# Performance work log

Hardware: AMD Instinct MI355X
Metric: run time of the kernel (lower is better)

The kernel has to match this reference:

```python
import jax, jax.numpy as jnp
import numpy as np

NUM_EXPERTS = 32
TOP_K = 8
SELECT_TOP_K = 4
THRESHOLD = 0.5
HIDDEN = 2048
D_FF = 768


def setup_inputs() -> dict:
    key = jax.random.key(0)
    ks = jax.random.split(key, 5)
    hidden_states = jax.random.normal(ks[0], (4, 2048, HIDDEN), dtype=jnp.float32)
    gate_weight = jax.random.normal(ks[1], (NUM_EXPERTS, HIDDEN), dtype=jnp.float32) * 0.02
    gate_up_proj = jax.random.normal(ks[2], (NUM_EXPERTS, 2 * D_FF, HIDDEN), dtype=jnp.float32) * 0.02
    down_proj = jax.random.normal(ks[3], (NUM_EXPERTS, HIDDEN, D_FF), dtype=jnp.float32) * 0.02
    similarity = jax.random.uniform(ks[4], (NUM_EXPERTS, NUM_EXPERTS), dtype=jnp.float32)
    return {
        "hidden_states": hidden_states,
        "gate_weight": gate_weight,
        "gate_up_proj": gate_up_proj,
        "down_proj": down_proj,
        "similarity": similarity,
    }


def _moe_forward(hidden_states, gate_weight, gate_up_proj, down_proj, similarity):
    B, S_len, H = hidden_states.shape
    E, K, Ssel = NUM_EXPERTS, TOP_K, SELECT_TOP_K
    x = hidden_states.reshape(-1, H)  # [T, H]

    # Router: logits -> fp32 softmax -> top-k -> renormalize
    router_logits = x @ gate_weight.T  # [T, E]
    router_probs = jax.nn.softmax(router_logits.astype(jnp.float32), axis=-1).astype(router_logits.dtype)
    router_top_value, router_indices = jax.lax.top_k(router_probs, K)  # [T, K]
    routing_weights = router_top_value / jnp.clip(
        jnp.sum(router_top_value, axis=-1, keepdims=True), 1e-12, None
    )

    # SERE rerouting: map each secondary expert to its most-similar primary expert
    sim = similarity.astype(jnp.float32)
    sim = sim.at[jnp.arange(E), jnp.arange(E)].set(1.0)  # fill_diagonal_(1.0)
    prim = router_indices[:, :Ssel]            # [T, S]
    sec = router_indices[:, Ssel:]             # [T, K-S]
    sim_cand = sim[sec[:, :, None], prim[:, None, :]]        # [T, K-S, S]
    best_sim = jnp.max(sim_cand, axis=-1)                    # [T, K-S]
    best_i = jnp.argmax(sim_cand, axis=-1)                   # [T, K-S]
    prim_rep = jnp.broadcast_to(prim[:, None, :], sim_cand.shape)
    best_primary = jnp.take_along_axis(prim_rep, best_i[..., None], axis=-1)[..., 0]
    new_sec = jnp.where(best_sim < THRESHOLD, sec, best_primary) if THRESHOLD > 0.0 else best_primary
    rerouted_indices = jnp.concatenate([prim, new_sec], axis=1)  # [T, K]

    # Combine weights per (token, expert); duplicate expert slots accumulate (index_add semantics)
    combine = jnp.sum(
        jax.nn.one_hot(rerouted_indices, E, dtype=routing_weights.dtype)
        * routing_weights[..., None],
        axis=1,
    )  # [T, E]

    # Dense masked expert sweep (scan over experts keeps peak memory at one [T, 2*D_FF] buffer)
    def expert_step(y, params):
        wgu, wd, cw = params  # [2F, H], [H, F], [T]
        gu = x @ wgu.T                      # [T, 2F]
        g, u = jnp.split(gu, 2, axis=-1)
        h = jax.nn.silu(g) * u              # SwiGLU
        y = y + (h @ wd.T) * cw[:, None]
        return y, None

    y0 = jnp.zeros_like(x)
    y, _ = jax.lax.scan(expert_step, y0, (gate_up_proj, down_proj, combine.T))
    return y.reshape(B, S_len, H)


def reference(hidden_states, gate_weight, gate_up_proj, down_proj, similarity):
    return _moe_forward(hidden_states, gate_weight, gate_up_proj, down_proj, similarity)
```

## Files before the change

### kernel.cpp

```cpp
#include <hip/hip_runtime.h>
#include <stdint.h>
#include <string.h>

#define NTOK 8192
#define HID 2048
#define NE 32
#define DFF 768
#define NSLOT 65536
#define NB 256
#define MT 256
#define MAX_TILES 288

typedef unsigned short u16;
typedef unsigned int u32;

using f32x4 = __attribute__((ext_vector_type(4))) float;
using bf16x8 = __attribute__((ext_vector_type(8))) short;

static __device__ __forceinline__ u16 f2bf(float f) {
  u32 x = __float_as_uint(f);
  x += 0x7fffu + ((x >> 16) & 1u);
  return (u16)(x >> 16);
}

typedef const __attribute__((address_space(1))) unsigned int* gp_t;
typedef __attribute__((address_space(3))) unsigned int* lp_t;
static __device__ __forceinline__ void gload16(const void* g, void* l) {
  __builtin_amdgcn_global_load_lds((gp_t)g, (lp_t)l, 16, 0, 0);
}

__global__ void convert2_kernel(const float* __restrict__ s1, u16* __restrict__ d1, int n1,
                                const float* __restrict__ s2, u16* __restrict__ d2, int n2) {
  int i = blockIdx.x * blockDim.x + threadIdx.x;
  int stride = gridDim.x * blockDim.x;
  int total = n1 + n2;
  for (; i < total; i += stride) {
    const float* src = (i < n1) ? s1 : s2;
    u16* dst = (i < n1) ? d1 : d2;
    int k = (i < n1) ? i : (i - n1);
    float4 v = reinterpret_cast<const float4*>(src)[k];
    u32 lo = (u32)f2bf(v.x) | ((u32)f2bf(v.y) << 16);
    u32 hi = (u32)f2bf(v.z) | ((u32)f2bf(v.w) << 16);
    reinterpret_cast<uint2*>(dst)[k] = make_uint2(lo, hi);
  }
}

__global__ void router_kernel(const float* __restrict__ x, const float* __restrict__ gw,
                              const float* __restrict__ sim,
                              int* __restrict__ slot_e, float* __restrict__ slot_w,
                              u16* __restrict__ xb) {
  int t = blockIdx.x;
  __shared__ float xs[HID];
  __shared__ float logits[NE];
  const float* xr = x + (size_t)t * HID;
  for (int i = threadIdx.x; i < HID / 4; i += 256)
    reinterpret_cast<float4*>(xs)[i] = reinterpret_cast<const float4*>(xr)[i];
  __syncthreads();
  {
    int i = threadIdx.x;
    float4 v0 = reinterpret_cast<float4*>(xs)[i * 2];
    float4 v1 = reinterpret_cast<float4*>(xs)[i * 2 + 1];
    uint4 o;
    o.x = (u32)f2bf(v0.x) | ((u32)f2bf(v0.y) << 16);
    o.y = (u32)f2bf(v0.z) | ((u32)f2bf(v0.w) << 16);
    o.z = (u32)f2bf(v1.x) | ((u32)f2bf(v1.y) << 16);
    o.w = (u32)f2bf(v1.z) | ((u32)f2bf(v1.w) << 16);
    reinterpret_cast<uint4*>(xb + (size_t)t * HID)[i] = o;
  }
  int e = threadIdx.x >> 3, part = threadIdx.x & 7;
  const float4* wv = reinterpret_cast<const float4*>(gw + (size_t)e * HID + part * 256);
  const float4* xv = reinterpret_cast<const float4*>(xs + part * 256);
  float s = 0.f;
#pragma unroll
  for (int j = 0; j < 64; ++j) {
    float4 a = xv[j], b = wv[j];
    s += a.x * b.x + a.y * b.y + a.z * b.z + a.w * b.w;
  }
  s += __shfl_xor(s, 1); s += __shfl_xor(s, 2); s += __shfl_xor(s, 4);
  if (part == 0) logits[e] = s;
  __syncthreads();
  if (threadIdx.x < 64) {
    int lane = threadIdx.x;
    float myv = (lane < NE) ? logits[lane] : -3.4e38f;
    int myi = lane;
    float cur = myv;
    int idx[8]; float lv[8];
#pragma unroll
    for (int k = 0; k < 8; ++k) {
      float bv = cur; int bi = myi;
#pragma unroll
      for (int off = 32; off; off >>= 1) {
        float ov = __shfl_xor(bv, off);
        int oi = __shfl_xor(bi, off);
        if (ov > bv || (ov == bv && oi < bi)) { bv = ov; bi = oi; }
      }
      idx[k] = bi; lv[k] = bv;
      if (myi == bi) cur = -3.4e38f;
    }
    float w[8]; float ssum = 0.f;
#pragma unroll
    for (int k = 0; k < 8; ++k) { w[k] = __expf(lv[k] - lv[0]); ssum += w[k]; }
    float inv = 1.f / ssum;
    int base = t * 8;
    if (lane < 4) {
      slot_e[base + lane] = idx[lane];
      slot_w[base + lane] = w[lane] * inv;
      int sj = idx[4 + lane];
      float best = -2.f; int bsel = idx[0];
#pragma unroll
      for (int i = 0; i < 4; ++i) {
        int pe = idx[i];
        float sv = sim[sj * NE + pe];
        bool ok = sv > best;
        best = ok ? sv : best;
        bsel = ok ? pe : bsel;
      }
      int ns = (best < 0.5f) ? sj : bsel;
      slot_e[base + 4 + lane] = ns;
      slot_w[base + 4 + lane] = w[4 + lane] * inv;
    }
  }
}

__global__ void hist_kernel(const int* __restrict__ slot_e, int* __restrict__ blockCounts) {
  __shared__ int cnt[NE];
  if (threadIdx.x < NE) cnt[threadIdx.x] = 0;
  __syncthreads();
  int i = blockIdx.x * 256 + threadIdx.x;
  atomicAdd(&cnt[slot_e[i]], 1);
  __syncthreads();
  if (threadIdx.x < NE) blockCounts[threadIdx.x * NB + blockIdx.x] = cnt[threadIdx.x];
}

__global__ void scan_kernel(const int* __restrict__ blockCounts, int* __restrict__ startEB,
                            int* __restrict__ tile_e, int* __restrict__ tile_row0,
                            int* __restrict__ tile_cnt, int* __restrict__ tileCount) {
  __shared__ int totals[NE];
  __shared__ int bases[NE];
  int t = threadIdx.x;
  if (t < NE) {
    int run = 0;
    for (int b = 0; b < NB; ++b) run += blockCounts[t * NB + b];
    totals[t] = run;
  }
  __syncthreads();
  if (t == 0) {
    int base = 0, nt = 0;
    for (int e = 0; e < NE; ++e) {
      bases[e] = base;
      int tot = totals[e];
      for (int i = 0; i < tot; i += MT) {
        tile_e[nt] = e;
        tile_row0[nt] = base + i;
        tile_cnt[nt] = (tot - i < MT) ? (tot - i) : MT;
        ++nt;
      }
      base += tot;
    }
    *tileCount = nt;
  }
  __syncthreads();
  if (t < NE) {
    int run = bases[t];
    for (int b = 0; b < NB; ++b) {
      startEB[t * NB + b] = run;
      run += blockCounts[t * NB + b];
    }
  }
}

__global__ void place_kernel(const int* __restrict__ slot_e, const float* __restrict__ slot_w,
                             const int* __restrict__ startEB,
                             int* __restrict__ perm_token, float* __restrict__ perm_w,
                             int* __restrict__ inv) {
  __shared__ int se[256];
  __shared__ float sw[256];
  int b = blockIdx.x;
  for (int i = threadIdx.x; i < 256; i += 64) {
    se[i] = slot_e[b * 256 + i];
    sw[i] = slot_w[b * 256 + i];
  }
  __syncthreads();
  int e = threadIdx.x;
  if (e < NE) {
    int pos = startEB[e * NB + b];
    for (int i = 0; i < 256; ++i) {
      if (se[i] == e) {
        perm_token[pos] = (b * 256 + i) >> 3;
        perm_w[pos] = sw[i];
        inv[b * 256 + i] = pos;
        ++pos;
      }
    }
  }
}


#define GUMM(AR, M_)                                                                   \
  acc[M_][0] = __builtin_amdgcn_mfma_f32_16x16x32_bf16(AR, b0, acc[M_][0], 0, 0, 0);   \
  acc[M_][1] = __builtin_amdgcn_mfma_f32_16x16x32_bf16(AR, b1, acc[M_][1], 0, 0, 0);   \
  acc[M_][2] = __builtin_amdgcn_mfma_f32_16x16x32_bf16(AR, b2, acc[M_][2], 0, 0, 0);   \
  acc[M_][3] = __builtin_amdgcn_mfma_f32_16x16x32_bf16(AR, b3, acc[M_][3], 0, 0, 0);

#define GWIN(BUF, KK, VM, S1, S2)                                                      \
  do {                                                                                 \
    asm volatile("s_waitcnt lgkmcnt(0)" ::: "memory");                                 \
    __builtin_amdgcn_sched_barrier(0);                                                 \
    asm volatile("s_waitcnt vmcnt(" #VM ")" ::: "memory");                             \
    __builtin_amdgcn_s_barrier();                                                      \
    const u16* Ap_ = &SA[BUF][KK][abase];                                              \
    const u16* Bp_ = &SB[BUF][KK][0];                                                  \
    bf16x8 a0_ = *(const bf16x8*)(Ap_);                                                \
    bf16x8 a1_ = *(const bf16x8*)(Ap_ + 512);                                          \
    bf16x8 a2_ = *(const bf16x8*)(Ap_ + 1024);                                         \
    bf16x8 a3_ = *(const bf16x8*)(Ap_ + 1536);                                         \
    bf16x8 b0 = *(const bf16x8*)(Bp_ + boff0);                                         \
    bf16x8 b1 = *(const bf16x8*)(Bp_ + boff1);                                         \
    bf16x8 b2 = *(const bf16x8*)(Bp_ + boff2);                                         \
    bf16x8 b3 = *(const bf16x8*)(Bp_ + boff3);                                         \
    S1;                                                                                \
    __builtin_amdgcn_s_setprio(1);                                                     \
    GUMM(a0_, 0) GUMM(a1_, 1) GUMM(a2_, 2) GUMM(a3_, 3)                                \
    __builtin_amdgcn_s_setprio(0);                                                     \
    bf16x8 c0_ = *(const bf16x8*)(Ap_ + 2048);                                         \
    bf16x8 c1_ = *(const bf16x8*)(Ap_ + 2560);                                         \
    bf16x8 c2_ = *(const bf16x8*)(Ap_ + 3072);                                         \
    bf16x8 c3_ = *(const bf16x8*)(Ap_ + 3584);                                         \
    S2;                                                                                \
    __builtin_amdgcn_s_setprio(1);                                                     \
    GUMM(c0_, 4) GUMM(c1_, 5) GUMM(c2_, 6) GUMM(c3_, 7)                                \
    __builtin_amdgcn_s_setprio(0);                                                     \
  } while (0)

__global__ __launch_bounds__(512, 2) void gu_fast(
    const u16* __restrict__ xb, const u16* __restrict__ wgub,
    const int* __restrict__ perm_token,
    const int* __restrict__ tile_e, const int* __restrict__ tile_row0,
    const int* __restrict__ tile_cnt, const int* __restrict__ tileCount,
    u16* __restrict__ h_perm) {
  int flat = blockIdx.x + blockIdx.y * 6;
  int xcd = flat & 7;
  int j = flat >> 3;
  int tile = xcd * 36 + j / 6;
  int n0g = (j % 6) * 128;
  if (tile >= *tileCount) return;
  int e = tile_e[tile], row0 = tile_row0[tile], cnt = tile_cnt[tile];
  __shared__ __align__(16) u16 SA[2][2][8192];
  __shared__ __align__(16) u16 SB[2][2][8192];
  __shared__ int toks[256];
  int tid = threadIdx.x;
  if (tid < 256) {
    int idx = row0 + tid;
    if (idx > NSLOT - 1) idx = NSLOT - 1;
    toks[tid] = perm_token[idx];
  }
  __syncthreads();
  int wave = tid >> 6, lane = tid & 63;
  int wr = wave >> 2, wc = wave & 3;
  int lr = lane & 15, lk = lane >> 4;
  int sr0 = tid >> 2;
  int sc0 = (tid & 3) ^ ((tid >> 3) & 3);
  const u16* gA0 = xb + (size_t)toks[sr0] * HID + sc0 * 8;
  const u16* gA1 = xb + (size_t)toks[128 + sr0] * HID + sc0 * 8;
  const u16* wgb = wgub + (size_t)e * (2 * DFF) * HID;
  const u16* gB0 = wgb + (size_t)(n0g + sr0) * HID + sc0 * 8;
  const u16* gB1 = wgb + (size_t)(DFF + n0g + sr0) * HID + sc0 * 8;
  int d0 = tid * 8, d1 = 4096 + tid * 8;

  int slot8 = (lk ^ ((lr >> 1) & 3)) * 8;
  int abase = (wr * 128 + lr) * 32 + slot8;
  int boff0 = (wc * 32 + 0 * 16 + lr) * 32 + slot8;
  int boff1 = (wc * 32 + 1 * 16 + lr) * 32 + slot8;
  int boff2 = (128 + wc * 32 + 0 * 16 + lr) * 32 + slot8;
  int boff3 = (128 + wc * 32 + 1 * 16 + lr) * 32 + slot8;

  f32x4 acc[8][4];
  f32x4 zero = {0.f, 0.f, 0.f, 0.f};
#pragma unroll
  for (int m = 0; m < 8; ++m)
#pragma unroll
    for (int n = 0; n < 4; ++n) acc[m][n] = zero;

#define GU_SGA(BUF, KK, KT) do { \
    gload16(gA0 + (KT) + (KK) * 32, &SA[BUF][KK][d0]); \
    gload16(gA1 + (KT) + (KK) * 32, &SA[BUF][KK][d1]); } while (0)
#define GU_SGB(BUF, KK, KT) do { \
    gload16(gB0 + (KT) + (KK) * 32, &SB[BUF][KK][d0]); \
    gload16(gB1 + (KT) + (KK) * 32, &SB[BUF][KK][d1]); } while (0)

  GU_SGA(0, 0, 0); GU_SGB(0, 0, 0);
  GU_SGA(0, 1, 0); GU_SGB(0, 1, 0);
  GU_SGA(1, 0, 64); GU_SGB(1, 0, 64);

  const int NKT = HID / 64;
  const int NI = NKT / 2;
  for (int it = 0; it < NI - 1; ++it) {
    int ktA = (2 * it + 1) * 64;
    int ktB = (2 * it + 2) * 64;
    int ktC = (2 * it + 3) * 64;
    GWIN(0, 0, 8, GU_SGA(1, 1, ktA), GU_SGB(1, 1, ktA));
    GWIN(0, 1, 8, GU_SGA(0, 0, ktB), GU_SGB(0, 0, ktB));
    GWIN(1, 0, 8, GU_SGA(0, 1, ktB), GU_SGB(0, 1, ktB));
    GWIN(1, 1, 8, GU_SGA(1, 0, ktC), GU_SGB(1, 0, ktC));
  }
  {
    int ktA = (2 * (NI - 1) + 1) * 64;
    GWIN(0, 0, 8, GU_SGA(1, 1, ktA), GU_SGB(1, 1, ktA));
    GWIN(0, 1, 8, (void)0, (void)0);
    GWIN(1, 0, 4, (void)0, (void)0);
    GWIN(1, 1, 0, (void)0, (void)0);
  }

#pragma unroll
  for (int m = 0; m < 8; ++m)
#pragma unroll
    for (int i = 0; i < 4; ++i) {
      int row = wr * 128 + m * 16 + lk * 4 + i;
      if (row < cnt) {
#pragma unroll
        for (int nf = 0; nf < 2; ++nf) {
          int col = n0g + wc * 32 + nf * 16 + lr;
          float g = acc[m][nf][i], u = acc[m][nf + 2][i];
          float h = g / (1.f + __expf(-g)) * u;
          h_perm[(size_t)(row0 + row) * DFF + col] = f2bf(h);
        }
      }
    }
#undef GU_SGA
#undef GU_SGB
}

__global__ __launch_bounds__(512, 2) void down_fast(
    const u16* __restrict__ h_perm, const u16* __restrict__ wdb,
    const float* __restrict__ perm_w,
    const int* __restrict__ tile_e, const int* __restrict__ tile_row0,
    const int* __restrict__ tile_cnt, const int* __restrict__ tileCount,
    _Float16* __restrict__ yp) {
  int flat = blockIdx.x + blockIdx.y * 8;
  int xcd = flat & 7;
  int j = flat >> 3;
  int tile = xcd * 36 + j / 8;
  int n0 = (j % 8) * 256;
  if (tile >= *tileCount) return;
  int e = tile_e[tile], row0 = tile_row0[tile], cnt = tile_cnt[tile];
  __shared__ __align__(16) u16 SA[2][2][8192];
  __shared__ __align__(16) u16 SB[2][2][8192];
  __shared__ float wts[256];
  int tid = threadIdx.x;
  if (tid < 256) {
    int idx = row0 + tid;
    if (idx > NSLOT - 1) idx = NSLOT - 1;
    wts[tid] = perm_w[idx];
  }
  __syncthreads();
  int wave = tid >> 6, lane = tid & 63;
  int wr = wave >> 2, wc = wave & 3;
  int lr = lane & 15, lk = lane >> 4;
  int sr0 = tid >> 2;
  int sc0 = (tid & 3) ^ ((tid >> 3) & 3);
  int ia0 = row0 + sr0;       if (ia0 > NSLOT - 1) ia0 = NSLOT - 1;
  int ia1 = row0 + 128 + sr0; if (ia1 > NSLOT - 1) ia1 = NSLOT - 1;
  const u16* gA0 = h_perm + (size_t)ia0 * DFF + sc0 * 8;
  const u16* gA1 = h_perm + (size_t)ia1 * DFF + sc0 * 8;
  const u16* wb = wdb + (size_t)e * HID * DFF;
  const u16* gB0 = wb + (size_t)(n0 + sr0) * DFF + sc0 * 8;
  const u16* gB1 = wb + (size_t)(n0 + 128 + sr0) * DFF + sc0 * 8;
  int d0 = tid * 8, d1 = 4096 + tid * 8;

  int slot8 = (lk ^ ((lr >> 1) & 3)) * 8;
  int abase = (wr * 128 + lr) * 32 + slot8;
  int boff0 = (wc * 64 + 0 * 16 + lr) * 32 + slot8;
  int boff1 = (wc * 64 + 1 * 16 + lr) * 32 + slot8;
  int boff2 = (wc * 64 + 2 * 16 + lr) * 32 + slot8;
  int boff3 = (wc * 64 + 3 * 16 + lr) * 32 + slot8;

  f32x4 acc[8][4];
  f32x4 zero = {0.f, 0.f, 0.f, 0.f};
#pragma unroll
  for (int m = 0; m < 8; ++m)
#pragma unroll
    for (int n = 0; n < 4; ++n) acc[m][n] = zero;

#define DN_SGA(BUF, KK, KT) do { \
    gload16(gA0 + (KT) + (KK) * 32, &SA[BUF][KK][d0]); \
    gload16(gA1 + (KT) + (KK) * 32, &SA[BUF][KK][d1]); } while (0)
#define DN_SGB(BUF, KK, KT) do { \
    gload16(gB0 + (KT) + (KK) * 32, &SB[BUF][KK][d0]); \
    gload16(gB1 + (KT) + (KK) * 32, &SB[BUF][KK][d1]); } while (0)

  DN_SGA(0, 0, 0); DN_SGB(0, 0, 0);
  DN_SGA(0, 1, 0); DN_SGB(0, 1, 0);
  DN_SGA(1, 0, 64); DN_SGB(1, 0, 64);

  const int NKT = DFF / 64;
  const int NI = NKT / 2;
  for (int it = 0; it < NI - 1; ++it) {
    int ktA = (2 * it + 1) * 64;
    int ktB = (2 * it + 2) * 64;
    int ktC = (2 * it + 3) * 64;
    GWIN(0, 0, 8, DN_SGA(1, 1, ktA), DN_SGB(1, 1, ktA));
    GWIN(0, 1, 8, DN_SGA(0, 0, ktB), DN_SGB(0, 0, ktB));
    GWIN(1, 0, 8, DN_SGA(0, 1, ktB), DN_SGB(0, 1, ktB));
    GWIN(1, 1, 8, DN_SGA(1, 0, ktC), DN_SGB(1, 0, ktC));
  }
  {
    int ktA = (2 * (NI - 1) + 1) * 64;
    GWIN(0, 0, 8, DN_SGA(1, 1, ktA), DN_SGB(1, 1, ktA));
    GWIN(0, 1, 8, (void)0, (void)0);
    GWIN(1, 0, 4, (void)0, (void)0);
    GWIN(1, 1, 0, (void)0, (void)0);
  }

#pragma unroll
  for (int m = 0; m < 8; ++m)
#pragma unroll
    for (int i = 0; i < 4; ++i) {
      int row = wr * 128 + m * 16 + lk * 4 + i;
      if (row < cnt) {
        float wt = wts[row];
#pragma unroll
        for (int nf = 0; nf < 4; ++nf) {
          int col = n0 + wc * 64 + nf * 16 + lr;
          yp[(size_t)(row0 + row) * HID + col] = (_Float16)(acc[m][nf][i] * wt);
        }
      }
    }
#undef DN_SGA
#undef DN_SGB
}

__global__ void reduce_kernel(const _Float16* __restrict__ yp, const int* __restrict__ inv,
                              float* __restrict__ y) {
  int t = blockIdx.x;
  __shared__ int pos[8];
  if (threadIdx.x < 8) pos[threadIdx.x] = inv[t * 8 + threadIdx.x];
  __syncthreads();
  int c = threadIdx.x * 8;
  float s[8] = {0.f, 0.f, 0.f, 0.f, 0.f, 0.f, 0.f, 0.f};
#pragma unroll
  for (int j = 0; j < 8; ++j) {
    uint4 v = *reinterpret_cast<const uint4*>(yp + (size_t)pos[j] * HID + c);
    const u16* p = reinterpret_cast<const u16*>(&v);
#pragma unroll
    for (int k = 0; k < 8; ++k) {
      _Float16 h;
      u16 us = p[k];
      __builtin_memcpy(&h, &us, 2);
      s[k] += (float)h;
    }
  }
  float* yo = y + (size_t)t * HID + c;
  float4 o0 = {s[0], s[1], s[2], s[3]};
  float4 o1 = {s[4], s[5], s[6], s[7]};
  *reinterpret_cast<float4*>(yo) = o0;
  *reinterpret_cast<float4*>(yo + 4) = o1;
}

extern "C" void kernel_launch(void* const* d_in, const int* in_sizes, int n_in,
                              void* d_out, int out_size, void* d_ws, size_t ws_size,
                              hipStream_t stream) {
  const float* x = (const float*)d_in[0];
  const float* gw = (const float*)d_in[1];
  const float* wgu = (const float*)d_in[2];
  const float* wd = (const float*)d_in[3];
  const float* sim = (const float*)d_in[4];
  float* y = (float*)d_out;

  char* ws = (char*)d_ws;
  size_t off = 0;
  auto alloc = [&](size_t bytes) {
    char* p = ws + off;
    off += (bytes + 255) & ~(size_t)255;
    return p;
  };
  u16* xb = (u16*)alloc((size_t)NTOK * HID * 2);
  u16* h_perm = (u16*)alloc((size_t)NSLOT * DFF * 2);
  int* slot_e = (int*)alloc(NSLOT * 4);
  float* slot_w = (float*)alloc(NSLOT * 4);
  int* perm_token = (int*)alloc(NSLOT * 4);
  float* perm_w = (float*)alloc(NSLOT * 4);
  int* inv = (int*)alloc(NSLOT * 4);
  int* blockCounts = (int*)alloc(NE * NB * 4);
  int* startEB = (int*)alloc(NE * NB * 4);
  int* tile_e = (int*)alloc(MAX_TILES * 4);
  int* tile_row0 = (int*)alloc(MAX_TILES * 4);
  int* tile_cnt = (int*)alloc(MAX_TILES * 4);
  int* tileCount = (int*)alloc(4);

  size_t wgu_elems = (size_t)NE * 2 * DFF * HID;
  size_t wd_elems = (size_t)NE * HID * DFF;
  size_t region_bytes = (size_t)NSLOT * HID * 2;
  u16* wd_b = (u16*)alloc(wd_elems * 2);
  char* region = alloc(region_bytes);
  u16* wgu_b = (u16*)region;
  _Float16* yp = (_Float16*)region;
  if (off > ws_size) return;

  router_kernel<<<NTOK, 256, 0, stream>>>(x, gw, sim, slot_e, slot_w, xb);
  hist_kernel<<<NB, 256, 0, stream>>>(slot_e, blockCounts);
  scan_kernel<<<1, 64, 0, stream>>>(blockCounts, startEB, tile_e, tile_row0, tile_cnt, tileCount);
  place_kernel<<<NB, 64, 0, stream>>>(slot_e, slot_w, startEB, perm_token, perm_w, inv);

  convert2_kernel<<<8192, 256, 0, stream>>>(wgu, wgu_b, (int)(wgu_elems / 4),
                                            wd, wd_b, (int)(wd_elems / 4));
  gu_fast<<<dim3(DFF / 128, MAX_TILES), 512, 0, stream>>>(
      xb, wgu_b, perm_token, tile_e, tile_row0, tile_cnt, tileCount, h_perm);
  down_fast<<<dim3(HID / 256, MAX_TILES), 512, 0, stream>>>(
      h_perm, wd_b, perm_w, tile_e, tile_row0, tile_cnt, tileCount, yp);
  reduce_kernel<<<NTOK, 256, 0, stream>>>(yp, inv, y);
}
```

Baseline: 1.205 ms.

## Fuse router, histogram and weight conversion into one kernel launch

Measured after the change: 1.211 ms. Within noise of the previous version (+0.5%).

```diff
diff --git a/kernel.cpp b/kernel.cpp
--- a/kernel.cpp
+++ b/kernel.cpp
@@ -10,6 +10,7 @@
 #define NB 256
 #define MT 256
 #define MAX_TILES 288
+#define CVT_BLOCKS 4096
 
 typedef unsigned short u16;
 typedef unsigned int u32;
@@ -29,29 +30,30 @@
   __builtin_amdgcn_global_load_lds((gp_t)g, (lp_t)l, 16, 0, 0);
 }
 
-__global__ void convert2_kernel(const float* __restrict__ s1, u16* __restrict__ d1, int n1,
-                                const float* __restrict__ s2, u16* __restrict__ d2, int n2) {
-  int i = blockIdx.x * blockDim.x + threadIdx.x;
-  int stride = gridDim.x * blockDim.x;
-  int total = n1 + n2;
-  for (; i < total; i += stride) {
-    const float* src = (i < n1) ? s1 : s2;
-    u16* dst = (i < n1) ? d1 : d2;
-    int k = (i < n1) ? i : (i - n1);
-    float4 v = reinterpret_cast<const float4*>(src)[k];
-    u32 lo = (u32)f2bf(v.x) | ((u32)f2bf(v.y) << 16);
-    u32 hi = (u32)f2bf(v.z) | ((u32)f2bf(v.w) << 16);
-    reinterpret_cast<uint2*>(dst)[k] = make_uint2(lo, hi);
-  }
-}
-
-__global__ void router_kernel(const float* __restrict__ x, const float* __restrict__ gw,
-                              const float* __restrict__ sim,
-                              int* __restrict__ slot_e, float* __restrict__ slot_w,
-                              u16* __restrict__ xb) {
-  int t = blockIdx.x;
+__global__ void router_convert_kernel(const float* __restrict__ x, const float* __restrict__ gw,
+                                      const float* __restrict__ sim,
+                                      int* __restrict__ slot_e, float* __restrict__ slot_w,
+                                      u16* __restrict__ xb, int* __restrict__ blockCounts,
+                                      const float* __restrict__ wgu, u16* __restrict__ wgu_b, int n1,
+                                      const float* __restrict__ wd, u16* __restrict__ wd_b, int n2) {
   __shared__ float xs[HID];
   __shared__ float logits[NE];
+  if (blockIdx.x >= NTOK) {
+    int i = (blockIdx.x - NTOK) * 256 + threadIdx.x;
+    int stride = CVT_BLOCKS * 256;
+    int total = n1 + n2;
+    for (; i < total; i += stride) {
+      const float* src = (i < n1) ? wgu : wd;
+      u16* dst = (i < n1) ? wgu_b : wd_b;
+      int k = (i < n1) ? i : (i - n1);
+      float4 v = reinterpret_cast<const float4*>(src)[k];
+      u32 lo = (u32)f2bf(v.x) | ((u32)f2bf(v.y) << 16);
+      u32 hi = (u32)f2bf(v.z) | ((u32)f2bf(v.w) << 16);
+      reinterpret_cast<uint2*>(dst)[k] = make_uint2(lo, hi);
+    }
+    return;
+  }
+  int t = blockIdx.x;
   const float* xr = x + (size_t)t * HID;
   for (int i = threadIdx.x; i < HID / 4; i += 256)
     reinterpret_cast<float4*>(xs)[i] = reinterpret_cast<const float4*>(xr)[i];
@@ -118,18 +120,10 @@
       int ns = (best < 0.5f) ? sj : bsel;
       slot_e[base + 4 + lane] = ns;
       slot_w[base + 4 + lane] = w[4 + lane] * inv;
-    }
-  }
-}
-
-__global__ void hist_kernel(const int* __restrict__ slot_e, int* __restrict__ blockCounts) {
-  __shared__ int cnt[NE];
-  if (threadIdx.x < NE) cnt[threadIdx.x] = 0;
-  __syncthreads();
-  int i = blockIdx.x * 256 + threadIdx.x;
-  atomicAdd(&cnt[slot_e[i]], 1);
-  __syncthreads();
-  if (threadIdx.x < NE) blockCounts[threadIdx.x * NB + blockIdx.x] = cnt[threadIdx.x];
+      atomicAdd(&blockCounts[idx[lane] * NB + (t >> 5)], 1);
+      atomicAdd(&blockCounts[ns * NB + (t >> 5)], 1);
+    }
+  }
 }
 
 __global__ void scan_kernel(const int* __restrict__ blockCounts, int* __restrict__ startEB,
@@ -496,13 +490,13 @@
   _Float16* yp = (_Float16*)region;
   if (off > ws_size) return;
 
-  router_kernel<<<NTOK, 256, 0, stream>>>(x, gw, sim, slot_e, slot_w, xb);
-  hist_kernel<<<NB, 256, 0, stream>>>(slot_e, blockCounts);
+  hipMemsetAsync(blockCounts, 0, NE * NB * 4, stream);
+  router_convert_kernel<<<NTOK + CVT_BLOCKS, 256, 0, stream>>>(
+      x, gw, sim, slot_e, slot_w, xb, blockCounts,
+      wgu, wgu_b, (int)(wgu_elems / 4), wd, wd_b, (int)(wd_elems / 4));
   scan_kernel<<<1, 64, 0, stream>>>(blockCounts, startEB, tile_e, tile_row0, tile_cnt, tileCount);
   place_kernel<<<NB, 64, 0, stream>>>(slot_e, slot_w, startEB, perm_token, perm_w, inv);
 
-  convert2_kernel<<<8192, 256, 0, stream>>>(wgu, wgu_b, (int)(wgu_elems / 4),
-                                            wd, wd_b, (int)(wd_elems / 4));
   gu_fast<<<dim3(DFF / 128, MAX_TILES), 512, 0, stream>>>(
       xb, wgu_b, perm_token, tile_e, tile_row0, tile_cnt, tileCount, h_perm);
   down_fast<<<dim3(HID / 256, MAX_TILES), 512, 0, stream>>>(
```
